# Performance work log

Measured on AMD Instinct MI355X. Metric: run time of the kernel, lower is better.

Reference implementation:

```python
import jax, jax.numpy as jnp
import numpy as np

# Static problem dims (match input_specs / init_kwargs)
B, NF, H, W = 4, 8, 512, 512
C = 8  # number of instance labels; all assumed present -> torch.unique == arange(C)
DELTA_V, DELTA_D = 0.5, 1.5
ALPHA, BETA, GAMMA = 1.0, 1.0, 0.001


def _safe_norm_from_sq(sq):
    # sqrt with zero-safe gradient (double-where trick)
    pos = sq > 0
    return jnp.where(pos, jnp.sqrt(jnp.where(pos, sq, 1.0)), 0.0)


def setup_inputs() -> dict:
    key = jax.random.key(0)
    k1, k2 = jax.random.split(key)
    prediction = jax.random.normal(k1, (B, NF, H, W), dtype=jnp.float32)
    target = jax.random.randint(k2, (B, H, W), 0, C).astype(jnp.int32)
    return {"prediction": prediction, "target": target}


def _per_sample_loss(pred, tgt):
    # pred: (NF, H, W) float, tgt: (H, W) int labels in [0, C)
    N = H * W
    p = pred.reshape(NF, N)                      # (NF, N)
    g = tgt.reshape(N)                           # (N,)
    onehot = (g[:, None] == jnp.arange(C)[None, :]).astype(p.dtype)  # (N, C)
    counts = onehot.sum(axis=0)                  # (C,) pixels per instance

    # per-instance means: sum(pred * mask) / count  -> (NF, C)
    sums = jnp.einsum('fn,nc->fc', p, onehot)
    means = sums / counts

    # l_var (faithful to original quirk: distance summed over ALL pixels &
    # clusters, then divided by each per-cluster count and summed):
    # diff = || (mu - pred) * mask || over feature dim
    diffvec = (means[:, None, :] - p[:, :, None]) * onehot[None, :, :]  # (NF, N, C)
    diff = _safe_norm_from_sq(jnp.sum(diffvec * diffvec, axis=0))       # (N, C)
    distance = jnp.clip(diff - DELTA_V, 0.0, 100000.0) ** 2
    l_var = (distance.sum() / counts).sum() / C

    # l_dist: pairwise inter-cluster margin
    m = means.T                                   # (C, NF)
    pd = m[:, None, :] - m[None, :, :]            # (C, C, NF)
    norm = _safe_norm_from_sq(jnp.sum(pd * pd, axis=2))  # (C, C)
    margin = 2.0 * DELTA_D * (1.0 - jnp.eye(C, dtype=p.dtype))
    l_dist = jnp.sum(jnp.clip(margin - norm, 0.0, 100000.0) ** 2) / (C * (C - 1))

    # l_reg
    l_reg = (_safe_norm_from_sq(jnp.sum(means * means, axis=0)) / C).sum()

    return ALPHA * l_var + BETA * l_dist + GAMMA * l_reg


def reference(prediction, target):
    losses = jax.vmap(_per_sample_loss)(prediction, target)  # (B,)
    return losses.sum() / B
```

## Files before the change

kernel.cpp:

```cpp
#include <hip/hip_runtime.h>

#define N_PIX (512*512)
#define NFEAT 8
#define NCLUS 8
#define NB    4
#define GRIDX 128
#define NCHUNK (N_PIX/4)
#define STRIDE (GRIDX*256)
#define PART_TOTAL (72*NB*GRIDX)
#define DIST_OFF  PART_TOTAL
#define S2_OFF    (DIST_OFF + NB*GRIDX)

__global__ __launch_bounds__(256) void k_sums(const float* __restrict__ pred,
                                              const int* __restrict__ tgt,
                                              float* __restrict__ ws) {
    const int tid = threadIdx.x;
    const int bx = blockIdx.x, b = blockIdx.y;
    const int lane = tid & 63, w = tid >> 6;

    float acc[64];
#pragma unroll
    for (int i = 0; i < 64; ++i) acc[i] = 0.0f;
    int cnt[8] = {0, 0, 0, 0, 0, 0, 0, 0};

    const int4*   t4 = (const int4*)(tgt + b * N_PIX);
    const float4* p4 = (const float4*)(pred + (size_t)b * NFEAT * N_PIX);

#pragma unroll
    for (int it = 0; it < NCHUNK / STRIDE; ++it) {
        const int i = bx * 256 + tid + it * STRIDE;
        int4 g4 = t4[i];
        int gs[4] = {g4.x, g4.y, g4.z, g4.w};
        float pr[NFEAT][4];
#pragma unroll
        for (int f = 0; f < NFEAT; ++f) {
            float4 v = p4[f * NCHUNK + i];
            pr[f][0] = v.x; pr[f][1] = v.y; pr[f][2] = v.z; pr[f][3] = v.w;
        }
#pragma unroll
        for (int j = 0; j < 4; ++j) {
            float m[NCLUS];
#pragma unroll
            for (int c = 0; c < NCLUS; ++c) {
                bool hit = (gs[j] == c);
                m[c] = hit ? 1.0f : 0.0f;
                cnt[c] += (int)__popcll(__ballot(hit));
            }
#pragma unroll
            for (int f = 0; f < NFEAT; ++f)
#pragma unroll
                for (int c = 0; c < NCLUS; ++c)
                    acc[f * 8 + c] = fmaf(m[c], pr[f][j], acc[f * 8 + c]);
        }
    }

#pragma unroll
    for (int k = 0; k < 6; ++k) {
        const int d = 1 << k;
        const int bit = (lane >> k) & 1;
#pragma unroll
        for (int p = 0; p < (64 >> 1); ++p) {
            if (p >= (64 >> (k + 1))) break;
            float a  = __shfl_xor(acc[2 * p],     d, 64);
            float bb = __shfl_xor(acc[2 * p + 1], d, 64);
            float own = bit ? acc[2 * p + 1] : acc[2 * p];
            float oth = bit ? bb : a;
            acc[p] = own + oth;
        }
    }

    __shared__ float ssum[4][64];
    __shared__ float scnt[4][8];
    ssum[w][lane] = acc[0];
    if (lane == 0) {
#pragma unroll
        for (int c = 0; c < NCLUS; ++c) scnt[w][c] = (float)cnt[c];
    }
    __syncthreads();

    if (tid < 72) {
        float s;
        if (tid < 64) s = ssum[0][tid] + ssum[1][tid] + ssum[2][tid] + ssum[3][tid];
        else { int c = tid - 64; s = scnt[0][c] + scnt[1][c] + scnt[2][c] + scnt[3][c]; }
        ws[tid * (NB * GRIDX) + b * GRIDX + bx] = s;
    }
}

__global__ __launch_bounds__(256) void k_var(const float* __restrict__ pred,
                                             const int* __restrict__ tgt,
                                             float* __restrict__ ws) {
    __shared__ float pp[72][4];
    __shared__ float raw[72];
    __shared__ float mean[NCLUS * 9];
    __shared__ float sl[4];
    const int tid = threadIdx.x;
    const int bx = blockIdx.x, b = blockIdx.y;

    for (int s = tid; s < 288; s += 256) {
        const int e = s >> 2, q = s & 3;
        const float4* src = (const float4*)(ws + e * (NB * GRIDX) + b * GRIDX) + q * 8;
        float4 a0 = src[0], a1 = src[1], a2 = src[2], a3 = src[3];
        float4 a4 = src[4], a5 = src[5], a6 = src[6], a7 = src[7];
        float r0 = (a0.x + a0.y + a0.z + a0.w) + (a1.x + a1.y + a1.z + a1.w);
        float r1 = (a2.x + a2.y + a2.z + a2.w) + (a3.x + a3.y + a3.z + a3.w);
        float r2 = (a4.x + a4.y + a4.z + a4.w) + (a5.x + a5.y + a5.z + a5.w);
        float r3 = (a6.x + a6.y + a6.z + a6.w) + (a7.x + a7.y + a7.z + a7.w);
        pp[e][q] = (r0 + r1) + (r2 + r3);
    }
    __syncthreads();
    if (tid < 72) {
        float s = (pp[tid][0] + pp[tid][1]) + (pp[tid][2] + pp[tid][3]);
        raw[tid] = s;
        if (bx == 0) ws[S2_OFF + b * 72 + tid] = s;
    }
    __syncthreads();
    if (tid < 64) {
        const int f = tid >> 3, c = tid & 7;
        mean[c * 9 + f] = raw[f * 8 + c] / raw[64 + c];
    }
    __syncthreads();

    const int4*   t4 = (const int4*)(tgt + b * N_PIX);
    const float4* p4 = (const float4*)(pred + (size_t)b * NFEAT * N_PIX);

    float local = 0.0f;
#pragma unroll
    for (int it = 0; it < NCHUNK / STRIDE; ++it) {
        const int i = bx * 256 + tid + it * STRIDE;
        int4 g4 = t4[i];
        int gs[4] = {g4.x, g4.y, g4.z, g4.w};
        float pr[NFEAT][4];
#pragma unroll
        for (int f = 0; f < NFEAT; ++f) {
            float4 v = p4[f * NCHUNK + i];
            pr[f][0] = v.x; pr[f][1] = v.y; pr[f][2] = v.z; pr[f][3] = v.w;
        }
#pragma unroll
        for (int j = 0; j < 4; ++j) {
            const float* m = &mean[gs[j] * 9];
            float dsq = 0.0f;
#pragma unroll
            for (int f = 0; f < NFEAT; ++f) {
                float d = m[f] - pr[f][j];
                dsq = fmaf(d, d, dsq);
            }
            float diff = sqrtf(dsq);
            float dm = fminf(fmaxf(diff - 0.5f, 0.0f), 100000.0f);
            local = fmaf(dm, dm, local);
        }
    }

#pragma unroll
    for (int o = 32; o >= 1; o >>= 1) local += __shfl_xor(local, o, 64);
    if ((tid & 63) == 0) sl[tid >> 6] = local;
    __syncthreads();
    if (tid == 0)
        ws[DIST_OFF + bx * NB + b] = sl[0] + sl[1] + sl[2] + sl[3];
}

__global__ __launch_bounds__(256) void k_final(const float* __restrict__ ws,
                                               float* __restrict__ out) {
    __shared__ float sd[256];
    __shared__ float meanL[NB][64];
    __shared__ float sl[NB];
    const int tid = threadIdx.x;

    sd[tid] = ws[DIST_OFF + tid] + ws[DIST_OFF + 256 + tid];
    __syncthreads();
#pragma unroll
    for (int off = 128; off >= 4; off >>= 1) {
        if (tid < off) sd[tid] += sd[tid + off];
        __syncthreads();
    }

    const int b = tid >> 6, idx = tid & 63;
    const float* S2 = ws + S2_OFF + b * 72;
    meanL[b][idx] = S2[idx] / S2[64 + (idx & 7)];
    __syncthreads();

    const int i = idx >> 3, j = idx & 7;
    float pdsq = 0.0f;
#pragma unroll
    for (int f = 0; f < 8; ++f) {
        float d = meanL[b][f * 8 + i] - meanL[b][f * 8 + j];
        pdsq = fmaf(d, d, pdsq);
    }
    float nrm = sqrtf(pdsq);
    float t = fminf(fmaxf(3.0f - nrm, 0.0f), 100000.0f);
    float val = (i == j) ? 0.0f : t * t * (1.0f / 56.0f);

    if (i == 0) {
        float rsq = 0.0f;
#pragma unroll
        for (int f = 0; f < 8; ++f) {
            float m = meanL[b][f * 8 + j];
            rsq = fmaf(m, m, rsq);
        }
        float invc = 1.0f / S2[64 + j];
        val += 0.001f * sqrtf(rsq) * 0.125f + sd[b] * invc * 0.125f;
    }

#pragma unroll
    for (int o = 32; o >= 1; o >>= 1) val += __shfl_xor(val, o, 64);
    if (idx == 0) sl[b] = val;
    __syncthreads();
    if (tid == 0) out[0] = (sl[0] + sl[1] + sl[2] + sl[3]) * 0.25f;
}

extern "C" void kernel_launch(void* const* d_in, const int* in_sizes, int n_in,
                              void* d_out, int out_size, void* d_ws, size_t ws_size,
                              hipStream_t stream) {
    const float* pred = (const float*)d_in[0];
    const int*   tgt  = (const int*)d_in[1];
    float* out = (float*)d_out;
    float* ws  = (float*)d_ws;

    dim3 grid(GRIDX, NB);
    k_sums<<<grid, 256, 0, stream>>>(pred, tgt, ws);
    k_var <<<grid, 256, 0, stream>>>(pred, tgt, ws);
    k_final<<<1, 256, 0, stream>>>(ws, out);
}
```

Before: 87.62 us.

## Pack labels to bytes for second pass and atomically reduce partials into replicas

The first pass now writes each group of four int32 labels as one packed 32-bit word to the workspace. The second pass reads these packed labels instead of the original int32 target, cutting label traffic in that pass by four. Per-block partial sums are now atomically added into 32 replica slots rather than 128 separate slots, so the second kernel's prologue reads less. This costs an extra memset launch, atomic contention, and a workspace write of the packed labels.

```diff
diff --git a/kernel.cpp b/kernel.cpp
--- a/kernel.cpp
+++ b/kernel.cpp
@@ -7,8 +7,11 @@
 #define GRIDX 128
 #define NCHUNK (N_PIX/4)
 #define STRIDE (GRIDX*256)
-#define PART_TOTAL (72*NB*GRIDX)
-#define DIST_OFF  PART_TOTAL
+#define NREP   32
+#define REP_SIZE  (72*NB*NREP)
+#define LBL_OFF   REP_SIZE
+#define LBL_SIZE  (NB*NCHUNK)
+#define DIST_OFF  (LBL_OFF + LBL_SIZE)
 #define S2_OFF    (DIST_OFF + NB*GRIDX)
 
 __global__ __launch_bounds__(256) void k_sums(const float* __restrict__ pred,
@@ -25,12 +28,15 @@
 
     const int4*   t4 = (const int4*)(tgt + b * N_PIX);
     const float4* p4 = (const float4*)(pred + (size_t)b * NFEAT * N_PIX);
+    unsigned int* lblw = (unsigned int*)ws + LBL_OFF + b * NCHUNK;
 
 #pragma unroll
     for (int it = 0; it < NCHUNK / STRIDE; ++it) {
         const int i = bx * 256 + tid + it * STRIDE;
         int4 g4 = t4[i];
         int gs[4] = {g4.x, g4.y, g4.z, g4.w};
+        lblw[i] = (unsigned int)g4.x | ((unsigned int)g4.y << 8) |
+                  ((unsigned int)g4.z << 16) | ((unsigned int)g4.w << 24);
         float pr[NFEAT][4];
 #pragma unroll
         for (int f = 0; f < NFEAT; ++f) {
@@ -82,12 +88,11 @@
         float s;
         if (tid < 64) s = ssum[0][tid] + ssum[1][tid] + ssum[2][tid] + ssum[3][tid];
         else { int c = tid - 64; s = scnt[0][c] + scnt[1][c] + scnt[2][c] + scnt[3][c]; }
-        ws[tid * (NB * GRIDX) + b * GRIDX + bx] = s;
+        unsafeAtomicAdd(&ws[tid * (NB * NREP) + b * NREP + (bx & (NREP - 1))], s);
     }
 }
 
 __global__ __launch_bounds__(256) void k_var(const float* __restrict__ pred,
-                                             const int* __restrict__ tgt,
                                              float* __restrict__ ws) {
     __shared__ float pp[72][4];
     __shared__ float raw[72];
@@ -98,14 +103,9 @@
 
     for (int s = tid; s < 288; s += 256) {
         const int e = s >> 2, q = s & 3;
-        const float4* src = (const float4*)(ws + e * (NB * GRIDX) + b * GRIDX) + q * 8;
-        float4 a0 = src[0], a1 = src[1], a2 = src[2], a3 = src[3];
-        float4 a4 = src[4], a5 = src[5], a6 = src[6], a7 = src[7];
-        float r0 = (a0.x + a0.y + a0.z + a0.w) + (a1.x + a1.y + a1.z + a1.w);
-        float r1 = (a2.x + a2.y + a2.z + a2.w) + (a3.x + a3.y + a3.z + a3.w);
-        float r2 = (a4.x + a4.y + a4.z + a4.w) + (a5.x + a5.y + a5.z + a5.w);
-        float r3 = (a6.x + a6.y + a6.z + a6.w) + (a7.x + a7.y + a7.z + a7.w);
-        pp[e][q] = (r0 + r1) + (r2 + r3);
+        const float4* src = (const float4*)(ws + e * (NB * NREP) + b * NREP) + q * 2;
+        float4 a0 = src[0], a1 = src[1];
+        pp[e][q] = (a0.x + a0.y + a0.z + a0.w) + (a1.x + a1.y + a1.z + a1.w);
     }
     __syncthreads();
     if (tid < 72) {
@@ -120,15 +120,14 @@
     }
     __syncthreads();
 
-    const int4*   t4 = (const int4*)(tgt + b * N_PIX);
+    const unsigned int* lblw = (const unsigned int*)ws + LBL_OFF + b * NCHUNK;
     const float4* p4 = (const float4*)(pred + (size_t)b * NFEAT * N_PIX);
 
     float local = 0.0f;
 #pragma unroll
     for (int it = 0; it < NCHUNK / STRIDE; ++it) {
         const int i = bx * 256 + tid + it * STRIDE;
-        int4 g4 = t4[i];
-        int gs[4] = {g4.x, g4.y, g4.z, g4.w};
+        unsigned int lb = lblw[i];
         float pr[NFEAT][4];
 #pragma unroll
         for (int f = 0; f < NFEAT; ++f) {
@@ -137,7 +136,7 @@
         }
 #pragma unroll
         for (int j = 0; j < 4; ++j) {
-            const float* m = &mean[gs[j] * 9];
+            const float* m = &mean[((lb >> (8 * j)) & 7u) * 9];
             float dsq = 0.0f;
 #pragma unroll
             for (int f = 0; f < NFEAT; ++f) {
@@ -215,8 +214,10 @@
     float* out = (float*)d_out;
     float* ws  = (float*)d_ws;
 
+    hipMemsetAsync(d_ws, 0, REP_SIZE * sizeof(float), stream);
+
     dim3 grid(GRIDX, NB);
     k_sums<<<grid, 256, 0, stream>>>(pred, tgt, ws);
-    k_var <<<grid, 256, 0, stream>>>(pred, tgt, ws);
+    k_var <<<grid, 256, 0, stream>>>(pred, ws);
     k_final<<<1, 256, 0, stream>>>(ws, out);
 }
```

New measurement: 88.45 us. No clear change (+0.9%).
